# Performance work log

Measured on AMD Instinct MI355X. Metric: run time of the kernel, lower is better.

## Reference

```python
import jax, jax.numpy as jnp
import numpy as np

# Module hyperparameters (from init_kwargs)
KH = KW = 3
STRIDE = 2
PAD = 1
OUT_PAD = 1
DIL = 1
IN_LEN = 8   # length of each input capsule
OUT_LEN = 8  # length of each output capsule
N_IN_CAPS = 64 // IN_LEN    # 8
N_OUT_CAPS = 64 // OUT_LEN  # 8
NUM_ITERATIONS = 3


def _squash(x):
    # v * |v|^2 / ((1 + |v|^2) * |v|), along last (capsule-length) dim
    sn = jnp.sum(x * x, axis=-1, keepdims=True)
    return x * (sn / ((1.0 + sn) * jnp.sqrt(sn + 1e-12)))


def _k_means_routing(priors, num_iterations):
    # priors: [..., K, M] ; soft k-means routing with 'dot' similarity,
    # softmax over the votes dim K (softmax_dim=-2), squash at the end.
    out = jnp.mean(priors, axis=-2, keepdims=True)          # [..., 1, M]
    for _ in range(num_iterations):
        nrm = jnp.linalg.norm(out, axis=-1, keepdims=True)
        out_n = out / jnp.maximum(nrm, 1e-12)               # F.normalize(p=2)
        logits = jnp.sum(priors * out_n, axis=-1, keepdims=True)  # [..., K, 1]
        probs = jax.nn.softmax(logits, axis=-2)
        out = jnp.sum(probs * priors, axis=-2, keepdims=True)
    return _squash(out)[..., 0, :]                          # [..., M]


def setup_inputs() -> dict:
    key = jax.random.key(0)
    k1, k2, k3 = jax.random.split(key, 3)
    input = jax.random.normal(k1, (2, 64, 32, 32), dtype=jnp.float32)
    # weight: (in_length, out_channels//out_length, out_length, kh, kw)
    weight = jax.random.normal(k2, (IN_LEN, N_OUT_CAPS, OUT_LEN, KH, KW), dtype=jnp.float32) * 0.1
    # bias: (out_channels//out_length, out_length)
    bias = jax.random.normal(k3, (N_OUT_CAPS, OUT_LEN), dtype=jnp.float32) * 0.1
    return {"input": input, "weight": weight, "bias": bias}


def reference(input, weight, bias):
    n, c_in, h_in, w_in = input.shape
    fi = c_in // IN_LEN
    fo = weight.shape[1]
    # conv_transpose == conv(lhs-dilated input, spatially flipped kernel)
    pad_lo = DIL * (KH - 1) - PAD
    patches = jax.lax.conv_general_dilated_patches(
        input, (KH, KW), (1, 1),
        padding=((pad_lo, pad_lo + OUT_PAD), (pad_lo, pad_lo + OUT_PAD)),
        lhs_dilation=(STRIDE, STRIDE), rhs_dilation=(DIL, DIL))
    ho, wo = patches.shape[-2], patches.shape[-1]
    # feature dim of patches is ordered (c, kh, kw), channel-major
    patches = patches.reshape(n, fi, IN_LEN, KH, KW, ho, wo)
    w_flip = weight[..., ::-1, ::-1]  # [IN_LEN, fo, OUT_LEN, KH, KW]
    # votes: each (input capsule, kernel tap) casts a vote per output capsule
    priors = jnp.einsum('nflhwpq,lgmhw->npqgfhwm', patches, w_flip)
    priors = priors.reshape(n, ho, wo, fo, fi * KH * KW, OUT_LEN)
    out = _k_means_routing(priors, NUM_ITERATIONS)  # [n, ho, wo, fo, OUT_LEN]
    out = out + bias                                # bias: [fo, OUT_LEN]
    out = out.reshape(n, ho, wo, fo * OUT_LEN).transpose(0, 3, 1, 2)
    return out  # [n, out_channels, ho, wo] = [2, 64, 64, 64]
```

## Files before the change

kernel.cpp:

```cpp
#include <hip/hip_runtime.h>
#include <math.h>

#define HIN 32
#define WIN 32
#define NITER 3

__global__ __launch_bounds__(256) void transpose_in(const float* __restrict__ in,
                                                    float* __restrict__ tin) {
    __shared__ float lds[64 * 33];
    const int t = threadIdx.x;
    const int n = blockIdx.x >> 5;
    const int s0 = (blockIdx.x & 31) << 5;
    const float* ib = in + n * 65536;
    float* ob = tin + n * 65536;
#pragma unroll
    for (int k = 0; k < 8; ++k) {
        int idx = k * 256 + t;
        int c = idx >> 5, sl = idx & 31;
        lds[c * 33 + sl] = ib[c * 1024 + s0 + sl];
    }
    __syncthreads();
#pragma unroll
    for (int k = 0; k < 8; ++k) {
        int idx = k * 256 + t;
        int sl = idx >> 6, c = idx & 63;
        ob[(size_t)(s0 + sl) * 64 + c] = lds[c * 33 + sl];
    }
}

template <int CTRL>
__device__ __forceinline__ float dpp_add(float v) {
    int p = __builtin_amdgcn_update_dpp(0, __float_as_int(v), CTRL, 0xF, 0xF, true);
    return v + __int_as_float(p);
}
__device__ __forceinline__ float sum8(float v) {
    v = dpp_add<0xB1>(v);
    v = dpp_add<0x4E>(v);
    v = dpp_add<0x141>(v);
    return v;
}

template <int TH, int TW>
__device__ __forceinline__ void run_path(
    const float* __restrict__ tin, const float* __restrict__ weight,
    const float* __restrict__ bias, float* __restrict__ out,
    float* __restrict__ wlds, float* __restrict__ olds,
    int t, int n, int p, int qb) {
    constexpr int T = TH * TW;
    constexpr float Z = (float)(72 - 8 * T);

    {
        const int g = (t >> 3) & 7;
        const int m = t & 7;
        const int mg = ((m + g) & 7) * 8;
        const int l0 = t >> 6;
#pragma unroll
        for (int k = 0; k < 2 * T; ++k) {
            const int vtap = k >> 1;
            const int chunk = k & 1;
            const int hh = (TH == 1) ? 1 : ((vtap / TW) * 2);
            const int ww = (TW == 1) ? 1 : ((vtap % TW) * 2);
            const int jflip = (2 - hh) * 3 + (2 - ww);
            const int l = chunk * 4 + l0;
            wlds[(vtap * 8 + g) * 68 + mg + l] =
                weight[(chunk * 256 + t) * 9 + jflip];
        }
    }
    __syncthreads();

    const int wave = t >> 6;
    const int lane = t & 63;
    const int g = lane >> 3;
    const int s = lane & 7;
    const int q = qb + 2 * wave;

    float pri[T][8];
#pragma unroll
    for (int i = 0; i < TH; ++i) {
        const int h = (TH == 1) ? 1 : i * 2;
        const int y = (p + h - 1) >> 1;
#pragma unroll
        for (int j = 0; j < TW; ++j) {
            const int v = i * TW + j;
            const int w = (TW == 1) ? 1 : j * 2;
            const int x = (q + w - 1) >> 1;
            const bool valid = (y < HIN) && (x < WIN);
            if (valid) {
                float xv[8];
                const float4* xp =
                    (const float4*)(tin + (((size_t)n * HIN + y) * WIN + x) * 64 + s * 8);
                float4 x0 = xp[0], x1 = xp[1];
                xv[0] = x0.x; xv[1] = x0.y; xv[2] = x0.z; xv[3] = x0.w;
                xv[4] = x1.x; xv[5] = x1.y; xv[6] = x1.z; xv[7] = x1.w;
                const float* wb = wlds + (v * 8 + g) * 68;
#pragma unroll
                for (int m = 0; m < 8; ++m) {
                    const float4* wp = (const float4*)(wb + ((m + g) & 7) * 8);
                    float4 w0 = wp[0], w1 = wp[1];
                    pri[v][m] = xv[0] * w0.x + xv[1] * w0.y + xv[2] * w0.z + xv[3] * w0.w +
                                xv[4] * w1.x + xv[5] * w1.y + xv[6] * w1.z + xv[7] * w1.w;
                }
            } else {
#pragma unroll
                for (int m = 0; m < 8; ++m) pri[v][m] = 0.f;
            }
        }
    }

    float o[8];
#pragma unroll
    for (int m = 0; m < 8; ++m) {
        float a = 0.f;
#pragma unroll
        for (int v = 0; v < T; ++v) a += pri[v][m];
        o[m] = sum8(a) * (1.f / 72.f);
    }

#pragma unroll
    for (int it = 0; it < NITER; ++it) {
        float sn = 0.f;
#pragma unroll
        for (int m = 0; m < 8; ++m) sn += o[m] * o[m];
        const float inv = __builtin_amdgcn_rsqf(fmaxf(sn, 1e-24f));
        float on[8];
#pragma unroll
        for (int m = 0; m < 8; ++m) on[m] = o[m] * inv;

        float r[9];
        r[8] = 0.f;
        float e[T];
#pragma unroll
        for (int v = 0; v < T; ++v) {
            float a = 0.f;
#pragma unroll
            for (int m = 0; m < 8; ++m) a += pri[v][m] * on[m];
            e[v] = __expf(a);
            r[8] += e[v];
        }
#pragma unroll
        for (int m = 0; m < 8; ++m) {
            float a = 0.f;
#pragma unroll
            for (int v = 0; v < T; ++v) a += e[v] * pri[v][m];
            r[m] = a;
        }
#pragma unroll
        for (int j = 0; j < 9; ++j) r[j] = sum8(r[j]);
        const float invs = __builtin_amdgcn_rcpf(r[8] + Z);
#pragma unroll
        for (int m = 0; m < 8; ++m) o[m] = r[m] * invs;
    }

    float sn = 0.f;
#pragma unroll
    for (int m = 0; m < 8; ++m) sn += o[m] * o[m];
    const float factor =
        sn * __builtin_amdgcn_rcpf(1.f + sn) * __builtin_amdgcn_rsqf(sn + 1e-12f);

    float val = o[0];
#pragma unroll
    for (int m = 1; m < 8; ++m)
        if (s == m) val = o[m];
    val = val * factor + bias[g * 8 + s];

    olds[lane * 5 + wave] = val;

    __syncthreads();
    const int c2 = t >> 2, w = t & 3;
    out[(((size_t)n * 64 + c2) * 64 + p) * 64 + qb + 2 * w] = olds[c2 * 5 + w];
}

__global__ __launch_bounds__(256) void caps_routing(
    const float* __restrict__ tin, const float* __restrict__ weight,
    const float* __restrict__ bias, float* __restrict__ out) {
    __shared__ float wlds[4 * 8 * 68];
    __shared__ float olds[64 * 5];
    const int t = threadIdx.x;

    const int b = blockIdx.x;
    const int n = b >> 10;
    const int p = (b >> 4) & 63;
    const int j = b & 15;
    const int qpar = j >> 3;
    const int qb = (j & 7) * 8 + qpar;

    if (p & 1) {
        if (qpar)
            run_path<2, 2>(tin, weight, bias, out, wlds, olds, t, n, p, qb);
        else
            run_path<2, 1>(tin, weight, bias, out, wlds, olds, t, n, p, qb);
    } else {
        if (qpar)
            run_path<1, 2>(tin, weight, bias, out, wlds, olds, t, n, p, qb);
        else
            run_path<1, 1>(tin, weight, bias, out, wlds, olds, t, n, p, qb);
    }
}

extern "C" void kernel_launch(void* const* d_in, const int* in_sizes, int n_in,
                              void* d_out, int out_size, void* d_ws, size_t ws_size,
                              hipStream_t stream) {
    const float* in = (const float*)d_in[0];
    const float* weight = (const float*)d_in[1];
    const float* bias = (const float*)d_in[2];
    float* out = (float*)d_out;
    float* tin = (float*)d_ws;

    transpose_in<<<64, 256, 0, stream>>>(in, tin);
    caps_routing<<<2048, 256, 0, stream>>>(tin, weight, bias, out);
}
```

Measured before the change: 74.36 us.

## Drop transpose kernel, read NCHW input directly, defer routing normalization

Removes the separate transpose kernel and has the routing kernel gather its 8 capsule channels straight from the NCHW input with strided scalar loads. This saves a launch and a workspace round trip, at the cost of less coalesced, non-vectorized input reads. It also defers the softmax-denominator division: the unnormalized sums are carried between iterations, since only the direction matters for the dot-product logits, and the division happens once at the end. Weight LDS padding goes from 68 to 64 floats per row, which may bring back bank conflicts.

```diff
diff --git a/kernel.cpp b/kernel.cpp
--- a/kernel.cpp
+++ b/kernel.cpp
@@ -4,29 +4,6 @@
 #define HIN 32
 #define WIN 32
 #define NITER 3
-
-__global__ __launch_bounds__(256) void transpose_in(const float* __restrict__ in,
-                                                    float* __restrict__ tin) {
-    __shared__ float lds[64 * 33];
-    const int t = threadIdx.x;
-    const int n = blockIdx.x >> 5;
-    const int s0 = (blockIdx.x & 31) << 5;
-    const float* ib = in + n * 65536;
-    float* ob = tin + n * 65536;
-#pragma unroll
-    for (int k = 0; k < 8; ++k) {
-        int idx = k * 256 + t;
-        int c = idx >> 5, sl = idx & 31;
-        lds[c * 33 + sl] = ib[c * 1024 + s0 + sl];
-    }
-    __syncthreads();
-#pragma unroll
-    for (int k = 0; k < 8; ++k) {
-        int idx = k * 256 + t;
-        int sl = idx >> 6, c = idx & 63;
-        ob[(size_t)(s0 + sl) * 64 + c] = lds[c * 33 + sl];
-    }
-}
 
 template <int CTRL>
 __device__ __forceinline__ float dpp_add(float v) {
@@ -42,7 +19,7 @@
 
 template <int TH, int TW>
 __device__ __forceinline__ void run_path(
-    const float* __restrict__ tin, const float* __restrict__ weight,
+    const float* __restrict__ in, const float* __restrict__ weight,
     const float* __restrict__ bias, float* __restrict__ out,
     float* __restrict__ wlds, float* __restrict__ olds,
     int t, int n, int p, int qb) {
@@ -50,9 +27,9 @@
     constexpr float Z = (float)(72 - 8 * T);
 
     {
-        const int g = (t >> 3) & 7;
-        const int m = t & 7;
-        const int mg = ((m + g) & 7) * 8;
+        const int sg = (t >> 3) & 7;
+        const int sm = t & 7;
+        const int smg = ((sm + sg) & 7) * 8;
         const int l0 = t >> 6;
 #pragma unroll
         for (int k = 0; k < 2 * T; ++k) {
@@ -62,7 +39,7 @@
             const int ww = (TW == 1) ? 1 : ((vtap % TW) * 2);
             const int jflip = (2 - hh) * 3 + (2 - ww);
             const int l = chunk * 4 + l0;
-            wlds[(vtap * 8 + g) * 68 + mg + l] =
+            wlds[(vtap * 8 + sg) * 64 + smg + l] =
                 weight[(chunk * 256 + t) * 9 + jflip];
         }
     }
@@ -74,6 +51,7 @@
     const int s = lane & 7;
     const int q = qb + 2 * wave;
 
+    const float* inbase = in + (size_t)(n * 64 + s * 8) * (HIN * WIN);
     float pri[T][8];
 #pragma unroll
     for (int i = 0; i < TH; ++i) {
@@ -87,12 +65,10 @@
             const bool valid = (y < HIN) && (x < WIN);
             if (valid) {
                 float xv[8];
-                const float4* xp =
-                    (const float4*)(tin + (((size_t)n * HIN + y) * WIN + x) * 64 + s * 8);
-                float4 x0 = xp[0], x1 = xp[1];
-                xv[0] = x0.x; xv[1] = x0.y; xv[2] = x0.z; xv[3] = x0.w;
-                xv[4] = x1.x; xv[5] = x1.y; xv[6] = x1.z; xv[7] = x1.w;
-                const float* wb = wlds + (v * 8 + g) * 68;
+#pragma unroll
+                for (int l = 0; l < 8; ++l)
+                    xv[l] = inbase[(l * HIN + y) * WIN + x];
+                const float* wb = wlds + (v * 8 + g) * 64;
 #pragma unroll
                 for (int m = 0; m < 8; ++m) {
                     const float4* wp = (const float4*)(wb + ((m + g) & 7) * 8);
@@ -107,27 +83,27 @@
         }
     }
 
-    float o[8];
+    float r[9];
 #pragma unroll
     for (int m = 0; m < 8; ++m) {
         float a = 0.f;
 #pragma unroll
         for (int v = 0; v < T; ++v) a += pri[v][m];
-        o[m] = sum8(a) * (1.f / 72.f);
+        r[m] = sum8(a);
     }
 
 #pragma unroll
     for (int it = 0; it < NITER; ++it) {
         float sn = 0.f;
 #pragma unroll
-        for (int m = 0; m < 8; ++m) sn += o[m] * o[m];
+        for (int m = 0; m < 8; ++m) sn += r[m] * r[m];
         const float inv = __builtin_amdgcn_rsqf(fmaxf(sn, 1e-24f));
         float on[8];
 #pragma unroll
-        for (int m = 0; m < 8; ++m) on[m] = o[m] * inv;
+        for (int m = 0; m < 8; ++m) on[m] = r[m] * inv;
 
-        float r[9];
-        r[8] = 0.f;
+        float acc[9];
+        acc[8] = 0.f;
         float e[T];
 #pragma unroll
         for (int v = 0; v < T; ++v) {
@@ -135,21 +111,23 @@
 #pragma unroll
             for (int m = 0; m < 8; ++m) a += pri[v][m] * on[m];
             e[v] = __expf(a);
-            r[8] += e[v];
+            acc[8] += e[v];
         }
 #pragma unroll
         for (int m = 0; m < 8; ++m) {
             float a = 0.f;
 #pragma unroll
             for (int v = 0; v < T; ++v) a += e[v] * pri[v][m];
-            r[m] = a;
+            acc[m] = a;
         }
 #pragma unroll
-        for (int j = 0; j < 9; ++j) r[j] = sum8(r[j]);
-        const float invs = __builtin_amdgcn_rcpf(r[8] + Z);
+        for (int j = 0; j < 9; ++j) r[j] = sum8(acc[j]);
+    }
+
+    const float invs = __builtin_amdgcn_rcpf(r[8] + Z);
+    float o[8];
 #pragma unroll
-        for (int m = 0; m < 8; ++m) o[m] = r[m] * invs;
-    }
+    for (int m = 0; m < 8; ++m) o[m] = r[m] * invs;
 
     float sn = 0.f;
 #pragma unroll
@@ -171,9 +149,9 @@
 }
 
 __global__ __launch_bounds__(256) void caps_routing(
-    const float* __restrict__ tin, const float* __restrict__ weight,
+    const float* __restrict__ in, const float* __restrict__ weight,
     const float* __restrict__ bias, float* __restrict__ out) {
-    __shared__ float wlds[4 * 8 * 68];
+    __shared__ float wlds[4 * 512];
     __shared__ float olds[64 * 5];
     const int t = threadIdx.x;
 
@@ -186,14 +164,14 @@
 
     if (p & 1) {
         if (qpar)
-            run_path<2, 2>(tin, weight, bias, out, wlds, olds, t, n, p, qb);
+            run_path<2, 2>(in, weight, bias, out, wlds, olds, t, n, p, qb);
         else
-            run_path<2, 1>(tin, weight, bias, out, wlds, olds, t, n, p, qb);
+            run_path<2, 1>(in, weight, bias, out, wlds, olds, t, n, p, qb);
     } else {
         if (qpar)
-            run_path<1, 2>(tin, weight, bias, out, wlds, olds, t, n, p, qb);
+            run_path<1, 2>(in, weight, bias, out, wlds, olds, t, n, p, qb);
         else
-            run_path<1, 1>(tin, weight, bias, out, wlds, olds, t, n, p, qb);
+            run_path<1, 1>(in, weight, bias, out, wlds, olds, t, n, p, qb);
     }
 }
 
@@ -204,8 +182,7 @@
     const float* weight = (const float*)d_in[1];
     const float* bias = (const float*)d_in[2];
     float* out = (float*)d_out;
-    float* tin = (float*)d_ws;
+    (void)d_ws; (void)ws_size;
 
-    transpose_in<<<64, 256, 0, stream>>>(in, tin);
-    caps_routing<<<2048, 256, 0, stream>>>(tin, weight, bias, out);
+    caps_routing<<<2048, 256, 0, stream>>>(in, weight, bias, out);
 }
```

Result: slower. 77.46 us (+4.2%).
